# Optimization experiments

Measured on AMD Instinct MI355X. Metric: run time of the kernel, lower is better.

Reference implementation:

```python
import jax, jax.numpy as jnp
import numpy as np

N = 500_000   # total nodes
B = 500       # number of graphs
C = 128       # channels


def setup_inputs() -> dict:
    key = jax.random.key(0)
    ks = jax.random.split(key, 10)
    node_embeddings = jax.random.normal(ks[0], (N, C), dtype=jnp.float32)
    latent_embeddings = jax.random.normal(ks[1], (B, C), dtype=jnp.float32)
    groups = jnp.sort(jax.random.randint(ks[2], (N,), 0, B)).astype(jnp.int32)
    # params (PyTorch Linear stored here as [in, out] matrices; same math)
    s = 1.0 / np.sqrt(C)
    attn_w = jax.random.normal(ks[3], (C, 1), dtype=jnp.float32) * s  # xavier-ish
    w_w = jax.random.normal(ks[4], (C, 1), dtype=jnp.float32) * s
    w_b = jnp.zeros((1,), dtype=jnp.float32)
    f1_w = jax.random.normal(ks[5], (C, C), dtype=jnp.float32) * s
    f1_b = jnp.zeros((C,), dtype=jnp.float32)
    f2_w = jax.random.normal(ks[6], (C, 1), dtype=jnp.float32) * s
    f2_b = jnp.zeros((1,), dtype=jnp.float32)
    return {
        "node_embeddings": node_embeddings,
        "latent_embeddings": latent_embeddings,
        "attn_w": attn_w, "w_w": w_w, "w_b": w_b,
        "f1_w": f1_w, "f1_b": f1_b, "f2_w": f2_w, "f2_b": f2_b,
        "groups": groups, "num_segments": B,
    }


def reference(node_embeddings, latent_embeddings, attn_w, w_w, w_b,
              f1_w, f1_b, f2_w, f2_b, groups, num_segments):
    # gather per-node context (faithful to original: indexes node table by graph id)
    ctx = node_embeddings[groups]            # [N, C]
    lat = latent_embeddings[groups]          # [N, C]
    alpha = jax.nn.sigmoid(ctx @ w_w + w_b)  # [N, 1]
    f_out = jax.nn.relu(lat @ f1_w + f1_b) @ f2_w + f2_b  # [N, 1]
    attn = alpha * f_out + (1.0 - alpha) * attn_w.T       # [N, C]
    scores = jnp.sum(node_embeddings * attn, axis=1, keepdims=True)  # [N, 1]
    scores = jnp.exp(scores - jnp.max(scores, axis=0, keepdims=True))
    denom = jax.ops.segment_sum(scores, groups, num_segments=num_segments)[groups]
    scores = scores / denom
    graph_embeddings = jax.ops.segment_sum(node_embeddings * scores, groups,
                                           num_segments=num_segments)  # [B, C]
    return graph_embeddings
```

## Files before the change

### kernel.cpp

```cpp
#include <hip/hip_runtime.h>
#include <math.h>

#define C 128
#define SPLIT 4
#define PSTRIDE (C + 4)

typedef float f32x4 __attribute__((ext_vector_type(4)));

__global__ void k_prep(const int* __restrict__ groups, int n, int b, int nbb,
                       const float* __restrict__ node,
                       const float* __restrict__ latent,
                       const float* __restrict__ attn_w,
                       const float* __restrict__ w_w,
                       const float* __restrict__ w_b,
                       const float* __restrict__ f1_w,
                       const float* __restrict__ f1_b,
                       const float* __restrict__ f2_w,
                       const float* __restrict__ f2_b,
                       int* __restrict__ start, float* __restrict__ attnv) {
    __shared__ float lds_lat[C];
    __shared__ float red[4];

    if ((int)blockIdx.x < nbb) {
        int i = blockIdx.x * blockDim.x + threadIdx.x;
        if (i >= n) return;
        int g = groups[i];
        int gp = (i == 0) ? -1 : groups[i - 1];
        for (int gg = gp + 1; gg <= g; ++gg) start[gg] = i;
        if (i == n - 1)
            for (int gg = g + 1; gg <= b; ++gg) start[gg] = n;
        return;
    }

    const int g = blockIdx.x - nbb;
    const int tid = threadIdx.x;
    const int lane = tid & 63;
    const int wv = tid >> 6;

    if (tid < C) lds_lat[tid] = latent[(size_t)g * C + tid];
    __syncthreads();
    if (tid < C) {
        float ap = node[(size_t)g * C + tid] * w_w[tid];
        float h0 = 0.f, h1 = 0.f;
        #pragma unroll 8
        for (int in = 0; in < C / 2; ++in)
            h0 = fmaf(lds_lat[in], f1_w[in * C + tid], h0);
        #pragma unroll 8
        for (int in = C / 2; in < C; ++in)
            h1 = fmaf(lds_lat[in], f1_w[in * C + tid], h1);
        float h = fmaxf(h0 + h1 + f1_b[tid], 0.f);
        float fp = h * f2_w[tid];
        #pragma unroll
        for (int off = 32; off >= 1; off >>= 1) {
            ap += __shfl_xor(ap, off);
            fp += __shfl_xor(fp, off);
        }
        if (lane == 0) { red[wv * 2] = ap; red[wv * 2 + 1] = fp; }
    }
    __syncthreads();
    if (tid < C) {
        float a_sum = red[0] + red[2];
        float f_sum = red[1] + red[3];
        float alpha = 1.f / (1.f + __expf(-(a_sum + w_b[0])));
        float fout = f_sum + f2_b[0];
        attnv[(size_t)g * C + tid] = alpha * fout + (1.f - alpha) * attn_w[tid];
    }
}

__global__ __launch_bounds__(256, 8)
void k_attn_part(const float* __restrict__ node,
                 const float* __restrict__ attnv,
                 const int* __restrict__ start,
                 float* __restrict__ part) {
    const int bid = blockIdx.x;
    const int g = bid >> 2;
    const int q = bid & 3;
    const int tid = threadIdx.x;
    const int lane = tid & 63;
    const int wv = tid >> 6;

    __shared__ float wacc[4][C];
    __shared__ float wm[4], wd[4];

    const int lo = start[g], hi = start[g + 1];
    const int len = hi - lo;
    const int s0 = lo + (len * q) / SPLIT;
    const int s1 = lo + (len * (q + 1)) / SPLIT;

    const int half = lane >> 5;
    const int cl = lane & 31;
    const f32x4 av = *(const f32x4*)&attnv[(size_t)g * C + cl * 4];

    float m = -INFINITY, denom = 0.f;
    f32x4 acc = (f32x4)(0.f);

    for (int base = s0 + wv * 8; base < s1; base += 32) {
        f32x4 r[4];
        #pragma unroll
        for (int j = 0; j < 4; ++j) {
            int row = base + 2 * j + half;
            int rc = row < s1 ? row : (s1 - 1);
            r[j] = *(const f32x4*)&node[(size_t)rc * C + cl * 4];
        }
        float s[4];
        #pragma unroll
        for (int j = 0; j < 4; ++j)
            s[j] = fmaf(r[j].x, av.x, fmaf(r[j].y, av.y,
                    fmaf(r[j].z, av.z, r[j].w * av.w)));

        float k0, k1;
        {
            float ka = (lane & 1) ? s[1] : s[0];
            float sa = (lane & 1) ? s[0] : s[1];
            float kb = (lane & 1) ? s[3] : s[2];
            float sb = (lane & 1) ? s[2] : s[3];
            k0 = ka + __shfl_xor(sa, 1);
            k1 = kb + __shfl_xor(sb, 1);
        }
        float k;
        {
            float ka = (lane & 2) ? k1 : k0;
            float sa = (lane & 2) ? k0 : k1;
            k = ka + __shfl_xor(sa, 2);
        }
        k += __shfl_xor(k, 4);
        k += __shfl_xor(k, 8);
        k += __shfl_xor(k, 16);
        int rown = base + 2 * (lane & 3) + half;
        k = (rown < s1) ? k : -INFINITY;

        float mx = k;
        mx = fmaxf(mx, __shfl_xor(mx, 1));
        mx = fmaxf(mx, __shfl_xor(mx, 2));
        mx = fmaxf(mx, __shfl_xor(mx, 32));
        float mb = fmaxf(m, mx);
        float scale = __expf(m - mb);
        float p = __expf(k - mb);

        float ps = p;
        ps += __shfl_xor(ps, 1);
        ps += __shfl_xor(ps, 2);
        ps += __shfl_xor(ps, 32);
        denom = fmaf(denom, scale, ps);

        float pe[4], po[4];
        #pragma unroll
        for (int t = 0; t < 4; ++t) {
            pe[t] = __shfl(p, t);
            po[t] = __shfl(p, 32 + t);
        }
        acc.x *= scale; acc.y *= scale; acc.z *= scale; acc.w *= scale;
        #pragma unroll
        for (int j = 0; j < 4; ++j) {
            float pj = half ? po[j] : pe[j];
            acc.x = fmaf(pj, r[j].x, acc.x);
            acc.y = fmaf(pj, r[j].y, acc.y);
            acc.z = fmaf(pj, r[j].z, acc.z);
            acc.w = fmaf(pj, r[j].w, acc.w);
        }
        m = mb;
    }

    acc.x += __shfl_xor(acc.x, 32);
    acc.y += __shfl_xor(acc.y, 32);
    acc.z += __shfl_xor(acc.z, 32);
    acc.w += __shfl_xor(acc.w, 32);

    if (lane == 0) { wm[wv] = m; wd[wv] = denom; }
    if (lane < 32) {
        wacc[wv][cl * 4 + 0] = acc.x;
        wacc[wv][cl * 4 + 1] = acc.y;
        wacc[wv][cl * 4 + 2] = acc.z;
        wacc[wv][cl * 4 + 3] = acc.w;
    }
    __syncthreads();

    if (tid < C) {
        float M = fmaxf(fmaxf(wm[0], wm[1]), fmaxf(wm[2], wm[3]));
        float D = 0.f, A = 0.f;
        #pragma unroll
        for (int w = 0; w < 4; ++w) {
            float sc = (wm[w] == -INFINITY) ? 0.f : __expf(wm[w] - M);
            D = fmaf(wd[w], sc, D);
            A = fmaf(wacc[w][tid], sc, A);
        }
        size_t pb = (size_t)bid * PSTRIDE;
        if (tid == 0) { part[pb] = M; part[pb + 1] = D; }
        part[pb + 4 + tid] = A;
    }
}

__global__ void k_merge(const float* __restrict__ part, float* __restrict__ out) {
    int g = blockIdx.x;
    int c = threadIdx.x;
    float M = -INFINITY;
    #pragma unroll
    for (int q = 0; q < SPLIT; ++q)
        M = fmaxf(M, part[(size_t)(g * SPLIT + q) * PSTRIDE]);
    float D = 0.f, A = 0.f;
    #pragma unroll
    for (int q = 0; q < SPLIT; ++q) {
        size_t pb = (size_t)(g * SPLIT + q) * PSTRIDE;
        float mq = part[pb];
        float sc = (mq == -INFINITY) ? 0.f : __expf(mq - M);
        D = fmaf(part[pb + 1], sc, D);
        A = fmaf(part[pb + 4 + c], sc, A);
    }
    out[(size_t)g * C + c] = (D > 0.f) ? (A / D) : 0.f;
}

extern "C" void kernel_launch(void* const* d_in, const int* in_sizes, int n_in,
                              void* d_out, int out_size, void* d_ws, size_t ws_size,
                              hipStream_t stream) {
    const float* node   = (const float*)d_in[0];
    const float* latent = (const float*)d_in[1];
    const float* attn_w = (const float*)d_in[2];
    const float* w_w    = (const float*)d_in[3];
    const float* w_b    = (const float*)d_in[4];
    const float* f1_w   = (const float*)d_in[5];
    const float* f1_b   = (const float*)d_in[6];
    const float* f2_w   = (const float*)d_in[7];
    const float* f2_b   = (const float*)d_in[8];
    const int*   groups = (const int*)d_in[9];

    const int n = in_sizes[9];
    const int b = in_sizes[1] / C;

    int*   start = (int*)d_ws;
    float* attnv = (float*)((char*)d_ws + 4096);
    float* part  = (float*)((char*)d_ws + 4096 + 1048576);

    const int nbb = (n + 255) / 256;
    k_prep<<<nbb + b, 256, 0, stream>>>(groups, n, b, nbb, node, latent,
                                        attn_w, w_w, w_b, f1_w, f1_b, f2_w, f2_b,
                                        start, attnv);
    k_attn_part<<<b * SPLIT, 256, 0, stream>>>(node, attnv, start, part);
    k_merge<<<b, C, 0, stream>>>(part, (float*)d_out);
}
```

Baseline: 53.48 us.

## Replace split-K partials and merge kernel with one 1024-thread block per graph

```diff
diff --git a/kernel.cpp b/kernel.cpp
--- a/kernel.cpp
+++ b/kernel.cpp
@@ -2,8 +2,7 @@
 #include <math.h>
 
 #define C 128
-#define SPLIT 4
-#define PSTRIDE (C + 4)
+#define NW 16
 
 typedef float f32x4 __attribute__((ext_vector_type(4)));
 
@@ -67,25 +66,20 @@
     }
 }
 
-__global__ __launch_bounds__(256, 8)
-void k_attn_part(const float* __restrict__ node,
-                 const float* __restrict__ attnv,
-                 const int* __restrict__ start,
-                 float* __restrict__ part) {
-    const int bid = blockIdx.x;
-    const int g = bid >> 2;
-    const int q = bid & 3;
+__global__ __launch_bounds__(1024, 8)
+void k_attn(const float* __restrict__ node,
+            const float* __restrict__ attnv,
+            const int* __restrict__ start,
+            float* __restrict__ out) {
+    const int g = blockIdx.x;
     const int tid = threadIdx.x;
     const int lane = tid & 63;
     const int wv = tid >> 6;
 
-    __shared__ float wacc[4][C];
-    __shared__ float wm[4], wd[4];
+    __shared__ float wacc[NW][C];
+    __shared__ float wm[NW], wd[NW];
 
     const int lo = start[g], hi = start[g + 1];
-    const int len = hi - lo;
-    const int s0 = lo + (len * q) / SPLIT;
-    const int s1 = lo + (len * (q + 1)) / SPLIT;
 
     const int half = lane >> 5;
     const int cl = lane & 31;
@@ -94,12 +88,12 @@
     float m = -INFINITY, denom = 0.f;
     f32x4 acc = (f32x4)(0.f);
 
-    for (int base = s0 + wv * 8; base < s1; base += 32) {
+    for (int base = lo + wv * 8; base < hi; base += NW * 8) {
         f32x4 r[4];
         #pragma unroll
         for (int j = 0; j < 4; ++j) {
             int row = base + 2 * j + half;
-            int rc = row < s1 ? row : (s1 - 1);
+            int rc = row < hi ? row : (hi - 1);
             r[j] = *(const f32x4*)&node[(size_t)rc * C + cl * 4];
         }
         float s[4];
@@ -127,7 +121,7 @@
         k += __shfl_xor(k, 8);
         k += __shfl_xor(k, 16);
         int rown = base + 2 * (lane & 3) + half;
-        k = (rown < s1) ? k : -INFINITY;
+        k = (rown < hi) ? k : -INFINITY;
 
         float mx = k;
         mx = fmaxf(mx, __shfl_xor(mx, 1));
@@ -176,37 +170,18 @@
     __syncthreads();
 
     if (tid < C) {
-        float M = fmaxf(fmaxf(wm[0], wm[1]), fmaxf(wm[2], wm[3]));
+        float M = -INFINITY;
+        #pragma unroll
+        for (int w = 0; w < NW; ++w) M = fmaxf(M, wm[w]);
         float D = 0.f, A = 0.f;
         #pragma unroll
-        for (int w = 0; w < 4; ++w) {
+        for (int w = 0; w < NW; ++w) {
             float sc = (wm[w] == -INFINITY) ? 0.f : __expf(wm[w] - M);
             D = fmaf(wd[w], sc, D);
             A = fmaf(wacc[w][tid], sc, A);
         }
-        size_t pb = (size_t)bid * PSTRIDE;
-        if (tid == 0) { part[pb] = M; part[pb + 1] = D; }
-        part[pb + 4 + tid] = A;
-    }
-}
-
-__global__ void k_merge(const float* __restrict__ part, float* __restrict__ out) {
-    int g = blockIdx.x;
-    int c = threadIdx.x;
-    float M = -INFINITY;
-    #pragma unroll
-    for (int q = 0; q < SPLIT; ++q)
-        M = fmaxf(M, part[(size_t)(g * SPLIT + q) * PSTRIDE]);
-    float D = 0.f, A = 0.f;
-    #pragma unroll
-    for (int q = 0; q < SPLIT; ++q) {
-        size_t pb = (size_t)(g * SPLIT + q) * PSTRIDE;
-        float mq = part[pb];
-        float sc = (mq == -INFINITY) ? 0.f : __expf(mq - M);
-        D = fmaf(part[pb + 1], sc, D);
-        A = fmaf(part[pb + 4 + c], sc, A);
-    }
-    out[(size_t)g * C + c] = (D > 0.f) ? (A / D) : 0.f;
+        out[(size_t)g * C + tid] = (D > 0.f) ? (A / D) : 0.f;
+    }
 }
 
 extern "C" void kernel_launch(void* const* d_in, const int* in_sizes, int n_in,
@@ -228,12 +203,10 @@
 
     int*   start = (int*)d_ws;
     float* attnv = (float*)((char*)d_ws + 4096);
-    float* part  = (float*)((char*)d_ws + 4096 + 1048576);
 
     const int nbb = (n + 255) / 256;
     k_prep<<<nbb + b, 256, 0, stream>>>(groups, n, b, nbb, node, latent,
                                         attn_w, w_w, w_b, f1_w, f1_b, f2_w, f2_b,
                                         start, attnv);
-    k_attn_part<<<b * SPLIT, 256, 0, stream>>>(node, attnv, start, part);
-    k_merge<<<b, C, 0, stream>>>(part, (float*)d_out);
+    k_attn<<<b, 1024, 0, stream>>>(node, attnv, start, (float*)d_out);
 }
```

After: 51.00 us. 4.6% less time.
